# Kernel optimization log

Measured on AMD Instinct MI355X. Metric: run time of the kernel, lower is better.

## Reference

```python
import jax, jax.numpy as jnp
import numpy as np

N, F_IN, F_OUT, K = 4096, 32, 32, 2
NEG_SLOPE = 0.2
MASK_VAL = -9e15


def _sparse_mat(kv, km, density=0.01):
    vals = jax.random.normal(kv, (N, N), dtype=jnp.float32)
    mask = jax.random.uniform(km, (N, N)) < density
    return vals * mask


def setup_inputs() -> dict:
    key = jax.random.key(0)
    ks = jax.random.split(key, 12)
    x = jax.random.normal(ks[0], (N, F_IN), dtype=jnp.float32)
    Ld = _sparse_mat(ks[1], ks[2])
    Lu = _sparse_mat(ks[3], ks[4])
    P = jax.random.normal(ks[5], (N, N), dtype=jnp.float32) / np.sqrt(N)
    W1 = jax.random.normal(ks[6], (K, F_IN, F_OUT), dtype=jnp.float32) * 0.1
    W2 = jax.random.normal(ks[7], (K, F_IN, F_OUT), dtype=jnp.float32) * 0.1
    W0 = jax.random.normal(ks[8], (F_IN, F_OUT), dtype=jnp.float32) * 0.1
    att1 = jax.random.normal(ks[9], (2 * F_OUT * K, 1), dtype=jnp.float32) * 0.1
    att2 = jax.random.normal(ks[10], (2 * F_OUT * K, 1), dtype=jnp.float32) * 0.1
    return {"x": x, "Ld": Ld, "Lu": Lu, "P": P, "W1": W1, "W2": W2,
            "W0": W0, "att1": att1, "att2": att2}


def _branch(x, L, W, att):
    # W: [K, F_in, F_out]; precompute x @ W[k] for all k -> [K, N, F_out]
    Kk, _, Fo = W.shape
    xw = jnp.einsum('nf,kfo->kno', x, W)
    # torch.cat([x@W[k]], dim=1) == transpose+reshape of xw
    xcat = jnp.transpose(xw, (1, 0, 2)).reshape(x.shape[0], Kk * Fo)
    d = Fo * Kk
    e = xcat @ att[:d] + (xcat @ att[d:]).T            # [N, N]
    e = jax.nn.leaky_relu(e, negative_slope=NEG_SLOPE)
    e = jnp.where(L != 0, e, MASK_VAL)
    alpha = jax.nn.softmax(e, axis=1)                   # row softmax, no dropout (eval)
    z = alpha @ xw[0]
    a = alpha
    for k in range(1, Kk):
        a = a @ L
        z = z + a @ xw[k]
    return z


def reference(x, Ld, Lu, P, W1, W2, W0, att1, att2):
    z1 = _branch(x, Ld, W1, att1)
    z2 = _branch(x, Lu, W2, att2)
    x0 = P @ (x @ W0)
    return z1 + z2 + x0
```

## Files before the change

### kernel.cpp

```cpp
#include <hip/hip_runtime.h>
#include <hip/hip_bf16.h>

#define NN 4096
#define CAP 128
#define KS 8

typedef __attribute__((ext_vector_type(8))) short bf16x8;
typedef __attribute__((ext_vector_type(4))) float f32x4;

__device__ __forceinline__ float lrelu(float v) { return v >= 0.f ? v : 0.2f * v; }

__device__ __forceinline__ ushort f2bu(float f) {
    unsigned u = __float_as_uint(f);
    return (ushort)((u + 0x7FFFu + ((u >> 16) & 1u)) >> 16);
}

__global__ __launch_bounds__(256) void k_prep(
    const float* __restrict__ x,
    const float* __restrict__ W1, const float* __restrict__ W2,
    const float* __restrict__ W0,
    const float* __restrict__ att1, const float* __restrict__ att2,
    float* __restrict__ xwA1, float* __restrict__ xwB1,
    float* __restrict__ xwA2, float* __restrict__ xwB2,
    float* __restrict__ a1, float* __restrict__ b1,
    float* __restrict__ a2, float* __restrict__ b2,
    __hip_bfloat16* __restrict__ Bt)
{
    __shared__ float wl[5120];
    __shared__ float xs[256];
    const int t = threadIdx.x;
    for (int i = t; i < 2048; i += 256) { wl[i] = W1[i]; wl[2048 + i] = W2[i]; }
    for (int i = t; i < 1024; i += 256) wl[4096 + i] = W0[i];
    const int rowBase = blockIdx.x * 8;
    xs[t] = x[rowBase * 32 + t];
    __syncthreads();

    const int o = t & 31, r = t >> 5;
    const int row = rowBase + r;
    const float* xr = &xs[r * 32];
    float vA1 = 0.f, vB1 = 0.f, vA2 = 0.f, vB2 = 0.f, v0 = 0.f;
#pragma unroll
    for (int f = 0; f < 32; ++f) {
        const float xv = xr[f];
        vA1 += xv * wl[f * 32 + o];
        vB1 += xv * wl[1024 + f * 32 + o];
        vA2 += xv * wl[2048 + f * 32 + o];
        vB2 += xv * wl[3072 + f * 32 + o];
        v0  += xv * wl[4096 + f * 32 + o];
    }
    xwA1[row * 32 + o] = vA1;
    xwB1[row * 32 + o] = vB1;
    xwA2[row * 32 + o] = vA2;
    xwB2[row * 32 + o] = vB2;
    ((ushort*)Bt)[(size_t)o * NN + row] = f2bu(v0);

    float pa1 = vA1 * att1[o]      + vB1 * att1[32 + o];
    float pb1 = vA1 * att1[64 + o] + vB1 * att1[96 + o];
    float pa2 = vA2 * att2[o]      + vB2 * att2[32 + o];
    float pb2 = vA2 * att2[64 + o] + vB2 * att2[96 + o];
#pragma unroll
    for (int m = 1; m <= 16; m <<= 1) {
        pa1 += __shfl_xor(pa1, m); pb1 += __shfl_xor(pb1, m);
        pa2 += __shfl_xor(pa2, m); pb2 += __shfl_xor(pb2, m);
    }
    if (o == 0) { a1[row] = pa1; b1[row] = pb1; a2[row] = pa2; b2[row] = pb2; }
}

__global__ __launch_bounds__(256) void k_csr2(
    const float* __restrict__ Ld, const float* __restrict__ Lu,
    int2* __restrict__ csrv, int* __restrict__ cntArr)
{
    const int r0 = blockIdx.x * 2;
    const int t = threadIdx.x, lane = t & 63, w = t >> 6;
    __shared__ int wcnt[16];

    float4 v[16];
    {
        const float4* A0 = (const float4*)(Ld + (size_t)r0 * NN);
        const float4* B0 = (const float4*)(Lu + (size_t)r0 * NN);
        const float4* A1 = (const float4*)(Ld + (size_t)(r0 + 1) * NN);
        const float4* B1 = (const float4*)(Lu + (size_t)(r0 + 1) * NN);
#pragma unroll
        for (int it = 0; it < 4; ++it) {
            v[it]      = A0[it * 256 + t];
            v[4 + it]  = B0[it * 256 + t];
            v[8 + it]  = A1[it * 256 + t];
            v[12 + it] = B1[it * 256 + t];
        }
    }

    const unsigned long long lt = (1ull << lane) - 1ull;
#pragma unroll
    for (int c = 0; c < 4; ++c) {
        const int row = r0 + (c >> 1);
        const int br  = c & 1;
        int2* out = csrv + ((size_t)br * NN + row) * CAP;
        int tots[4];
#pragma unroll
        for (int it = 0; it < 4; ++it) {
            const float4 fv = v[c * 4 + it];
            tots[it] = __popcll(__ballot(fv.x != 0.f)) + __popcll(__ballot(fv.y != 0.f))
                     + __popcll(__ballot(fv.z != 0.f)) + __popcll(__ballot(fv.w != 0.f));
        }
        __syncthreads();
        if (lane == 0) {
            int4 tv; tv.x = tots[0]; tv.y = tots[1]; tv.z = tots[2]; tv.w = tots[3];
            *(int4*)&wcnt[w * 4] = tv;
        }
        __syncthreads();
        const int4 ca = *(const int4*)&wcnt[0];
        const int4 cb = *(const int4*)&wcnt[4];
        const int4 cc = *(const int4*)&wcnt[8];
        const int4 cd = *(const int4*)&wcnt[12];
        const int cs[16] = {ca.x, ca.y, ca.z, ca.w, cb.x, cb.y, cb.z, cb.w,
                            cc.x, cc.y, cc.z, cc.w, cd.x, cd.y, cd.z, cd.w};
        int total = 0;
#pragma unroll
        for (int k2 = 0; k2 < 16; ++k2) total += cs[k2];
        int base = 0;
#pragma unroll
        for (int k2 = 0; k2 < 16; ++k2) base += (k2 < (w << 2)) ? cs[k2] : 0;
        const int cnt  = min(total, CAP);
        const int cp16 = min((cnt + 15) & ~15, CAP);

#pragma unroll
        for (int it = 0; it < 4; ++it) {
            const float4 fv = v[c * 4 + it];
            const unsigned long long m0 = __ballot(fv.x != 0.f);
            const unsigned long long m1 = __ballot(fv.y != 0.f);
            const unsigned long long m2 = __ballot(fv.z != 0.f);
            const unsigned long long m3 = __ballot(fv.w != 0.f);
            const int p0 = __popcll(m0), p1 = __popcll(m1), p2 = __popcll(m2);
            const int c0 = (it * 256 + t) * 4;
            int s;
            s = base + __popcll(m0 & lt);
            if (fv.x != 0.f && s < CAP) { int2 e; e.x = c0;     e.y = __float_as_int(fv.x); out[s] = e; }
            s = base + p0 + __popcll(m1 & lt);
            if (fv.y != 0.f && s < CAP) { int2 e; e.x = c0 + 1; e.y = __float_as_int(fv.y); out[s] = e; }
            s = base + p0 + p1 + __popcll(m2 & lt);
            if (fv.z != 0.f && s < CAP) { int2 e; e.x = c0 + 2; e.y = __float_as_int(fv.z); out[s] = e; }
            s = base + p0 + p1 + p2 + __popcll(m3 & lt);
            if (fv.w != 0.f && s < CAP) { int2 e; e.x = c0 + 3; e.y = __float_as_int(fv.w); out[s] = e; }
            base += p0 + p1 + p2 + __popcll(m3);
        }
        if (t >= cnt && t < cp16) { int2 e; e.x = 0; e.y = 0; out[t] = e; }
        if (t == 0) cntArr[br * NN + row] = cnt;
    }
}

__global__ __launch_bounds__(256) void k_gather2(
    int2* __restrict__ csrv, const int* __restrict__ cntArr,
    const float* __restrict__ xwB1, const float* __restrict__ xwB2,
    const float* __restrict__ xwA1, const float* __restrict__ xwA2,
    const float* __restrict__ a1, const float* __restrict__ b1,
    const float* __restrict__ a2, const float* __restrict__ b2,
    float* __restrict__ u1, float* __restrict__ u2)
{
    __shared__ int2 sle[4][CAP];
    const int w = threadIdx.x >> 6, lane = threadIdx.x & 63;
    const int row = blockIdx.x * 4 + w;
    const int br  = blockIdx.y;
    const float* xwB = br ? xwB2 : xwB1;
    const float* xwA = br ? xwA2 : xwA1;
    const float* aA  = br ? a2 : a1;
    const float* bA  = br ? b2 : b1;
    float* u = br ? u2 : u1;

    const int cnt  = cntArr[br * NN + row];
    const int cp16 = min((cnt + 15) & ~15, CAP);
    int2* ci = csrv + ((size_t)br * NN + row) * CAP;
    int2* se = sle[w];
    int2 l0 = {0, 0}, l1 = {0, 0};
    if (lane < cp16)      { l0 = ci[lane];      se[lane]      = l0; }
    if (lane + 64 < cp16) { l1 = ci[lane + 64]; se[lane + 64] = l1; }

    const float ai = aA[row];
    const float e0 = (lane < cnt)      ? lrelu(ai + bA[l0.x]) : -1e30f;
    const float e1 = (lane + 64 < cnt) ? lrelu(ai + bA[l1.x]) : -1e30f;
    float lmax = fmaxf(e0, e1);
#pragma unroll
    for (int m = 1; m <= 32; m <<= 1) lmax = fmaxf(lmax, __shfl_xor(lmax, m));
    const float w0 = __expf(e0 - lmax), w1 = __expf(e1 - lmax);
    float ssum = w0 + w1;
#pragma unroll
    for (int m = 1; m <= 32; m <<= 1) ssum += __shfl_xor(ssum, m);
    const float inv = (cnt > 0) ? 1.f / ssum : 0.f;
    if (lane < cp16)      { l0.y = __float_as_int((lane < cnt)      ? w0 * inv : 0.f); ci[lane]      = l0; }
    if (lane + 64 < cp16) { l1.y = __float_as_int((lane + 64 < cnt) ? w1 * inv : 0.f); ci[lane + 64] = l1; }

    const int o = lane & 31, g = lane >> 5;
    float acc = 0.f;
    const int nb = cp16 >> 3;
    for (int j = 0; j < nb; ++j) {
        float wv[4], xv[4];
#pragma unroll
        for (int q = 0; q < 4; ++q) {
            const int2 e = se[8 * j + 2 * q + g];
            wv[q] = __int_as_float(e.y);
            xv[q] = xwB[(size_t)e.x * 32 + o];
        }
#pragma unroll
        for (int q = 0; q < 4; ++q) acc += wv[q] * xv[q];
    }
    acc += __shfl_xor(acc, 32);
    if (lane < 32) u[(size_t)row * 32 + o] = acc + xwA[(size_t)row * 32 + o];
}

__global__ __launch_bounds__(256) void k_accum(
    const int2* __restrict__ csrv, const int* __restrict__ cntArr,
    const float* __restrict__ u1, const float* __restrict__ u2,
    const float* __restrict__ partial, float* __restrict__ outp)
{
    __shared__ int2 sle[4][2 * CAP];
    const int w = threadIdx.x >> 6, lane = threadIdx.x & 63;
    const int row = blockIdx.x * 4 + w;
    const int o = lane & 31, g = lane >> 5;
    int2* se = sle[w];
    float total = 0.f;

    int cp[2];
#pragma unroll
    for (int br = 0; br < 2; ++br) {
        const int cnt = cntArr[br * NN + row];
        cp[br] = min((cnt + 15) & ~15, CAP);
        const int2* ci = csrv + ((size_t)br * NN + row) * CAP;
        if (lane < cp[br])      se[br * CAP + lane]      = ci[lane];
        if (lane + 64 < cp[br]) se[br * CAP + lane + 64] = ci[lane + 64];
    }

#pragma unroll
    for (int br = 0; br < 2; ++br) {
        const float* U = br ? u2 : u1;
        float acc = 0.f;
        const int nb = cp[br] >> 3;
        for (int j = 0; j < nb; ++j) {
            float wv[4], uv[4];
#pragma unroll
            for (int q = 0; q < 4; ++q) {
                const int2 e = se[br * CAP + 8 * j + 2 * q + g];
                wv[q] = __int_as_float(e.y);
                uv[q] = U[(size_t)e.x * 32 + o];
            }
#pragma unroll
            for (int q = 0; q < 4; ++q) acc += wv[q] * uv[q];
        }
        acc += __shfl_xor(acc, 32);
        total += acc;
    }

    if (lane < 32) {
#pragma unroll
        for (int p = 0; p < KS; ++p)
            total += partial[(size_t)p * NN * 32 + (size_t)row * 32 + o];
        outp[(size_t)row * 32 + o] = total;
    }
}

__global__ __launch_bounds__(256) void k_pgemm(
    const float* __restrict__ P, const ushort* __restrict__ Bt,
    float* __restrict__ partial)
{
    __shared__ ushort sA[2][16 * 64 * 8];
    __shared__ ushort sB[2][8 * 64 * 8];
    const int t = threadIdx.x;
    const int row0 = blockIdx.x * 64;
    const int ks = blockIdx.y;
    const float4*  P4  = (const float4*)P;
    const ushort4* Bt4 = (const ushort4*)Bt;

    const int lane = t & 63, w = t >> 6;

    f32x4 acc0 = {0.f, 0.f, 0.f, 0.f};
    f32x4 acc1 = {0.f, 0.f, 0.f, 0.f};

    auto stageA = [&](int c, int buf) {
        const int kc4 = (ks * 512 + c * 128) >> 2;
#pragma unroll
        for (int j = 0; j < 8; ++j) {
            const int i = t + 256 * j;
            const int row = i >> 5, q = i & 31;
            const float4 v = P4[(size_t)(row0 + row) * 1024 + kc4 + q];
            ushort4 u;
            u.x = f2bu(v.x); u.y = f2bu(v.y); u.z = f2bu(v.z); u.w = f2bu(v.w);
            const int wi = row >> 4, m = row & 15;
            const int kk = q >> 3, quad = (q >> 1) & 3, jj = q & 1;
            *(ushort4*)&sA[buf][(((wi * 4 + kk) * 64) + quad * 16 + m) * 8 + jj * 4] = u;
        }
    };
    auto stageB = [&](int c, int buf) {
        const int kc4 = (ks * 512 + c * 128) >> 2;
#pragma unroll
        for (int j = 0; j < 4; ++j) {
            const int i = t + 256 * j;
            const int o = i >> 5, q = i & 31;
            const ushort4 u = Bt4[(size_t)o * 1024 + kc4 + q];
            const int nt = o >> 4, n = o & 15;
            const int kk = q >> 3, quad = (q >> 1) & 3, jj = q & 1;
            *(ushort4*)&sB[buf][(((kk * 2 + nt) * 64) + quad * 16 + n) * 8 + jj * 4] = u;
        }
    };
    auto compute = [&](int buf) {
        const ushort* pa = &sA[buf][(w * 4) * 64 * 8 + lane * 8];
        const ushort* pb = &sB[buf][lane * 8];
#pragma unroll
        for (int kk = 0; kk < 4; ++kk) {
            const bf16x8 a  = *(const bf16x8*)(pa + kk * 512);
            const bf16x8 b0 = *(const bf16x8*)(pb + kk * 1024);
            const bf16x8 b1 = *(const bf16x8*)(pb + kk * 1024 + 512);
            acc0 = __builtin_amdgcn_mfma_f32_16x16x32_bf16(a, b0, acc0, 0, 0, 0);
            acc1 = __builtin_amdgcn_mfma_f32_16x16x32_bf16(a, b1, acc1, 0, 0, 0);
        }
    };

    stageA(0, 0); stageB(0, 0);
    __syncthreads();
    for (int c = 0; c < 4; ++c) {
        if (c < 3) { stageA(c + 1, (c + 1) & 1); stageB(c + 1, (c + 1) & 1); }
        compute(c & 1);
        __syncthreads();
    }

    const int m = lane & 15, quad = lane >> 4;
    float* out = partial + ((size_t)ks * NN + row0 + w * 16 + quad * 4) * 32;
#pragma unroll
    for (int r = 0; r < 4; ++r) {
        out[r * 32 + m]      = acc0[r];
        out[r * 32 + 16 + m] = acc1[r];
    }
}

extern "C" void kernel_launch(void* const* d_in, const int* in_sizes, int n_in,
                              void* d_out, int out_size, void* d_ws, size_t ws_size,
                              hipStream_t stream) {
    (void)in_sizes; (void)n_in; (void)out_size; (void)ws_size;
    const float* x    = (const float*)d_in[0];
    const float* Ld   = (const float*)d_in[1];
    const float* Lu   = (const float*)d_in[2];
    const float* P    = (const float*)d_in[3];
    const float* W1   = (const float*)d_in[4];
    const float* W2   = (const float*)d_in[5];
    const float* W0   = (const float*)d_in[6];
    const float* att1 = (const float*)d_in[7];
    const float* att2 = (const float*)d_in[8];

    float* ws = (float*)d_ws;
    float* xwA1 = ws;
    float* xwB1 = ws + 131072;
    float* xwA2 = ws + 262144;
    float* xwB2 = ws + 393216;
    float* u1   = ws + 524288;
    float* u2   = ws + 655360;
    float* a1   = ws + 786432;
    float* b1   = ws + 790528;
    float* a2   = ws + 794624;
    float* b2   = ws + 798720;
    float* partial = ws + 802816;
    __hip_bfloat16* Bt = (__hip_bfloat16*)(ws + 1851392);
    int2* csrv = (int2*)(ws + 1916928);
    int*  cnt  = (int*)(ws + 4014080);

    k_prep<<<512, 256, 0, stream>>>(x, W1, W2, W0, att1, att2,
                                    xwA1, xwB1, xwA2, xwB2, a1, b1, a2, b2, Bt);
    k_csr2<<<NN / 2, 256, 0, stream>>>(Ld, Lu, csrv, cnt);
    k_pgemm<<<dim3(64, KS), 256, 0, stream>>>(P, (const ushort*)Bt, partial);
    k_gather2<<<dim3(NN / 4, 2), 256, 0, stream>>>(csrv, cnt, xwB1, xwB2,
                                                   xwA1, xwA2, a1, b1, a2, b2,
                                                   u1, u2);
    k_accum<<<NN / 4, 256, 0, stream>>>(csrv, cnt, u1, u2, partial,
                                        (float*)d_out);
}
```

Baseline: 236.9 us.

## Fuse CSR compaction with softmax and gather into a single per-row kernel

```diff
diff --git a/kernel.cpp b/kernel.cpp
--- a/kernel.cpp
+++ b/kernel.cpp
@@ -66,144 +66,139 @@
     if (o == 0) { a1[row] = pa1; b1[row] = pb1; a2[row] = pa2; b2[row] = pb2; }
 }
 
-__global__ __launch_bounds__(256) void k_csr2(
+__global__ __launch_bounds__(256) void k_scan3(
     const float* __restrict__ Ld, const float* __restrict__ Lu,
-    int2* __restrict__ csrv, int* __restrict__ cntArr)
-{
-    const int r0 = blockIdx.x * 2;
-    const int t = threadIdx.x, lane = t & 63, w = t >> 6;
-    __shared__ int wcnt[16];
-
-    float4 v[16];
-    {
-        const float4* A0 = (const float4*)(Ld + (size_t)r0 * NN);
-        const float4* B0 = (const float4*)(Lu + (size_t)r0 * NN);
-        const float4* A1 = (const float4*)(Ld + (size_t)(r0 + 1) * NN);
-        const float4* B1 = (const float4*)(Lu + (size_t)(r0 + 1) * NN);
-#pragma unroll
-        for (int it = 0; it < 4; ++it) {
-            v[it]      = A0[it * 256 + t];
-            v[4 + it]  = B0[it * 256 + t];
-            v[8 + it]  = A1[it * 256 + t];
-            v[12 + it] = B1[it * 256 + t];
-        }
-    }
-
-    const unsigned long long lt = (1ull << lane) - 1ull;
-#pragma unroll
-    for (int c = 0; c < 4; ++c) {
-        const int row = r0 + (c >> 1);
-        const int br  = c & 1;
-        int2* out = csrv + ((size_t)br * NN + row) * CAP;
-        int tots[4];
-#pragma unroll
-        for (int it = 0; it < 4; ++it) {
-            const float4 fv = v[c * 4 + it];
-            tots[it] = __popcll(__ballot(fv.x != 0.f)) + __popcll(__ballot(fv.y != 0.f))
-                     + __popcll(__ballot(fv.z != 0.f)) + __popcll(__ballot(fv.w != 0.f));
-        }
-        __syncthreads();
-        if (lane == 0) {
-            int4 tv; tv.x = tots[0]; tv.y = tots[1]; tv.z = tots[2]; tv.w = tots[3];
-            *(int4*)&wcnt[w * 4] = tv;
-        }
-        __syncthreads();
-        const int4 ca = *(const int4*)&wcnt[0];
-        const int4 cb = *(const int4*)&wcnt[4];
-        const int4 cc = *(const int4*)&wcnt[8];
-        const int4 cd = *(const int4*)&wcnt[12];
-        const int cs[16] = {ca.x, ca.y, ca.z, ca.w, cb.x, cb.y, cb.z, cb.w,
-                            cc.x, cc.y, cc.z, cc.w, cd.x, cd.y, cd.z, cd.w};
-        int total = 0;
-#pragma unroll
-        for (int k2 = 0; k2 < 16; ++k2) total += cs[k2];
-        int base = 0;
-#pragma unroll
-        for (int k2 = 0; k2 < 16; ++k2) base += (k2 < (w << 2)) ? cs[k2] : 0;
-        const int cnt  = min(total, CAP);
-        const int cp16 = min((cnt + 15) & ~15, CAP);
-
-#pragma unroll
-        for (int it = 0; it < 4; ++it) {
-            const float4 fv = v[c * 4 + it];
-            const unsigned long long m0 = __ballot(fv.x != 0.f);
-            const unsigned long long m1 = __ballot(fv.y != 0.f);
-            const unsigned long long m2 = __ballot(fv.z != 0.f);
-            const unsigned long long m3 = __ballot(fv.w != 0.f);
-            const int p0 = __popcll(m0), p1 = __popcll(m1), p2 = __popcll(m2);
-            const int c0 = (it * 256 + t) * 4;
-            int s;
-            s = base + __popcll(m0 & lt);
-            if (fv.x != 0.f && s < CAP) { int2 e; e.x = c0;     e.y = __float_as_int(fv.x); out[s] = e; }
-            s = base + p0 + __popcll(m1 & lt);
-            if (fv.y != 0.f && s < CAP) { int2 e; e.x = c0 + 1; e.y = __float_as_int(fv.y); out[s] = e; }
-            s = base + p0 + p1 + __popcll(m2 & lt);
-            if (fv.z != 0.f && s < CAP) { int2 e; e.x = c0 + 2; e.y = __float_as_int(fv.z); out[s] = e; }
-            s = base + p0 + p1 + p2 + __popcll(m3 & lt);
-            if (fv.w != 0.f && s < CAP) { int2 e; e.x = c0 + 3; e.y = __float_as_int(fv.w); out[s] = e; }
-            base += p0 + p1 + p2 + __popcll(m3);
-        }
-        if (t >= cnt && t < cp16) { int2 e; e.x = 0; e.y = 0; out[t] = e; }
-        if (t == 0) cntArr[br * NN + row] = cnt;
-    }
-}
-
-__global__ __launch_bounds__(256) void k_gather2(
-    int2* __restrict__ csrv, const int* __restrict__ cntArr,
     const float* __restrict__ xwB1, const float* __restrict__ xwB2,
     const float* __restrict__ xwA1, const float* __restrict__ xwA2,
     const float* __restrict__ a1, const float* __restrict__ b1,
     const float* __restrict__ a2, const float* __restrict__ b2,
+    int2* __restrict__ csrv, int* __restrict__ cntArr,
     float* __restrict__ u1, float* __restrict__ u2)
 {
-    __shared__ int2 sle[4][CAP];
-    const int w = threadIdx.x >> 6, lane = threadIdx.x & 63;
-    const int row = blockIdx.x * 4 + w;
+    const int row = blockIdx.x;
     const int br  = blockIdx.y;
+    const float* L   = br ? Lu : Ld;
     const float* xwB = br ? xwB2 : xwB1;
     const float* xwA = br ? xwA2 : xwA1;
     const float* aA  = br ? a2 : a1;
     const float* bA  = br ? b2 : b1;
-    float* u = br ? u2 : u1;
-
-    const int cnt  = cntArr[br * NN + row];
+    int2* csrB = csrv + ((size_t)br * NN + row) * CAP;
+    float* u   = br ? u2 : u1;
+
+    __shared__ int   sidx[CAP];
+    __shared__ float sval[CAP];
+    __shared__ int   wcnt[16];
+    __shared__ float red[256];
+    __shared__ float rpart[8];
+    const int t = threadIdx.x;
+    const int lane = t & 63, w = t >> 6;
+
+    const float4* L4 = (const float4*)(L + (size_t)row * NN);
+    float4 v[4];
+#pragma unroll
+    for (int it = 0; it < 4; ++it) v[it] = L4[it * 256 + t];
+
+    const unsigned long long lt = (1ull << lane) - 1ull;
+
+    int tots[4];
+#pragma unroll
+    for (int it = 0; it < 4; ++it) {
+        const unsigned long long m0 = __ballot(v[it].x != 0.f);
+        const unsigned long long m1 = __ballot(v[it].y != 0.f);
+        const unsigned long long m2 = __ballot(v[it].z != 0.f);
+        const unsigned long long m3 = __ballot(v[it].w != 0.f);
+        tots[it] = __popcll(m0) + __popcll(m1) + __popcll(m2) + __popcll(m3);
+    }
+    if (lane == 0) {
+        int4 tv; tv.x = tots[0]; tv.y = tots[1]; tv.z = tots[2]; tv.w = tots[3];
+        *(int4*)&wcnt[w * 4] = tv;
+    }
+    __syncthreads();
+
+    const int4 ca = *(const int4*)&wcnt[0];
+    const int4 cb = *(const int4*)&wcnt[4];
+    const int4 cc = *(const int4*)&wcnt[8];
+    const int4 cd = *(const int4*)&wcnt[12];
+    const int cs[16] = {ca.x, ca.y, ca.z, ca.w, cb.x, cb.y, cb.z, cb.w,
+                        cc.x, cc.y, cc.z, cc.w, cd.x, cd.y, cd.z, cd.w};
+    int total = 0;
+#pragma unroll
+    for (int k2 = 0; k2 < 16; ++k2) total += cs[k2];
+    int base = 0;
+#pragma unroll
+    for (int k2 = 0; k2 < 16; ++k2) base += (k2 < (w << 2)) ? cs[k2] : 0;
+
+    const int cnt  = min(total, CAP);
     const int cp16 = min((cnt + 15) & ~15, CAP);
-    int2* ci = csrv + ((size_t)br * NN + row) * CAP;
-    int2* se = sle[w];
-    int2 l0 = {0, 0}, l1 = {0, 0};
-    if (lane < cp16)      { l0 = ci[lane];      se[lane]      = l0; }
-    if (lane + 64 < cp16) { l1 = ci[lane + 64]; se[lane + 64] = l1; }
+
+#pragma unroll
+    for (int it = 0; it < 4; ++it) {
+        const float vx = v[it].x, vy = v[it].y, vz = v[it].z, vw = v[it].w;
+        const unsigned long long m0 = __ballot(vx != 0.f);
+        const unsigned long long m1 = __ballot(vy != 0.f);
+        const unsigned long long m2 = __ballot(vz != 0.f);
+        const unsigned long long m3 = __ballot(vw != 0.f);
+        const int p0 = __popcll(m0), p1 = __popcll(m1), p2 = __popcll(m2);
+        const int c0 = (it * 256 + t) * 4;
+        int s;
+        s = base + __popcll(m0 & lt);
+        if (vx != 0.f && s < CAP) { sidx[s] = c0;     sval[s] = vx; }
+        s = base + p0 + __popcll(m1 & lt);
+        if (vy != 0.f && s < CAP) { sidx[s] = c0 + 1; sval[s] = vy; }
+        s = base + p0 + p1 + __popcll(m2 & lt);
+        if (vz != 0.f && s < CAP) { sidx[s] = c0 + 2; sval[s] = vz; }
+        s = base + p0 + p1 + p2 + __popcll(m3 & lt);
+        if (vw != 0.f && s < CAP) { sidx[s] = c0 + 3; sval[s] = vw; }
+        base += p0 + p1 + p2 + __popcll(m3);
+    }
+    if (t >= cnt && t < cp16) { sidx[t] = 0; sval[t] = 0.f; }
+    __syncthreads();
 
     const float ai = aA[row];
-    const float e0 = (lane < cnt)      ? lrelu(ai + bA[l0.x]) : -1e30f;
-    const float e1 = (lane + 64 < cnt) ? lrelu(ai + bA[l1.x]) : -1e30f;
-    float lmax = fmaxf(e0, e1);
-#pragma unroll
-    for (int m = 1; m <= 32; m <<= 1) lmax = fmaxf(lmax, __shfl_xor(lmax, m));
-    const float w0 = __expf(e0 - lmax), w1 = __expf(e1 - lmax);
-    float ssum = w0 + w1;
-#pragma unroll
-    for (int m = 1; m <= 32; m <<= 1) ssum += __shfl_xor(ssum, m);
+    const int myidx = (t < cp16) ? sidx[t] : 0;
+    const float e = (t < cnt) ? lrelu(ai + bA[myidx]) : -1e30f;
+    float m = e;
+#pragma unroll
+    for (int mm = 1; mm <= 32; mm <<= 1) m = fmaxf(m, __shfl_xor(m, mm));
+    if (lane == 0) rpart[w] = m;
+    __syncthreads();
+    m = fmaxf(fmaxf(rpart[0], rpart[1]), fmaxf(rpart[2], rpart[3]));
+    const float wgt = (t < cnt) ? __expf(e - m) : 0.f;
+    float ss = wgt;
+#pragma unroll
+    for (int mm = 1; mm <= 32; mm <<= 1) ss += __shfl_xor(ss, mm);
+    if (lane == 0) rpart[4 + w] = ss;
+    __syncthreads();
+    const float ssum = rpart[4] + rpart[5] + rpart[6] + rpart[7];
     const float inv = (cnt > 0) ? 1.f / ssum : 0.f;
-    if (lane < cp16)      { l0.y = __float_as_int((lane < cnt)      ? w0 * inv : 0.f); ci[lane]      = l0; }
-    if (lane + 64 < cp16) { l1.y = __float_as_int((lane + 64 < cnt) ? w1 * inv : 0.f); ci[lane + 64] = l1; }
-
-    const int o = lane & 31, g = lane >> 5;
+    if (t < cp16) { int2 eo; eo.x = myidx; eo.y = __float_as_int(wgt * inv); csrB[t] = eo; }
+    if (t == 0) cntArr[br * NN + row] = cnt;
+
+    const int o = t & 31, g = t >> 5;
     float acc = 0.f;
-    const int nb = cp16 >> 3;
-    for (int j = 0; j < nb; ++j) {
-        float wv[4], xv[4];
-#pragma unroll
-        for (int q = 0; q < 4; ++q) {
-            const int2 e = se[8 * j + 2 * q + g];
-            wv[q] = __int_as_float(e.y);
-            xv[q] = xwB[(size_t)e.x * 32 + o];
-        }
-#pragma unroll
-        for (int q = 0; q < 4; ++q) acc += wv[q] * xv[q];
-    }
-    acc += __shfl_xor(acc, 32);
-    if (lane < 32) u[(size_t)row * 32 + o] = acc + xwA[(size_t)row * 32 + o];
+    const int nPair = cp16 >> 4;
+    if (nPair > 0) {
+        float vA0 = sval[g],      vA1 = sval[g + 8];
+        float xA0 = xwB[(size_t)sidx[g] * 32 + o];
+        float xA1 = xwB[(size_t)sidx[g + 8] * 32 + o];
+        for (int j = 1; j < nPair; ++j) {
+            const int sB = g + 16 * j;
+            const float vB0 = sval[sB],  vB1 = sval[sB + 8];
+            const float xB0 = xwB[(size_t)sidx[sB] * 32 + o];
+            const float xB1 = xwB[(size_t)sidx[sB + 8] * 32 + o];
+            acc += vA0 * xA0 + vA1 * xA1;
+            vA0 = vB0; xA0 = xB0; vA1 = vB1; xA1 = xB1;
+        }
+        acc += vA0 * xA0 + vA1 * xA1;
+    }
+    red[t] = acc;
+    __syncthreads();
+    if (t < 32) {
+        float tot2 = 0.f;
+#pragma unroll
+        for (int g2 = 0; g2 < 8; ++g2) tot2 += red[g2 * 32 + t];
+        u[(size_t)row * 32 + t] = tot2 + xwA[(size_t)row * 32 + t];
+    }
 }
 
 __global__ __launch_bounds__(256) void k_accum(
@@ -361,11 +356,9 @@
 
     k_prep<<<512, 256, 0, stream>>>(x, W1, W2, W0, att1, att2,
                                     xwA1, xwB1, xwA2, xwB2, a1, b1, a2, b2, Bt);
-    k_csr2<<<NN / 2, 256, 0, stream>>>(Ld, Lu, csrv, cnt);
+    k_scan3<<<dim3(NN, 2), 256, 0, stream>>>(Ld, Lu, xwB1, xwB2, xwA1, xwA2,
+                                             a1, b1, a2, b2, csrv, cnt, u1, u2);
     k_pgemm<<<dim3(64, KS), 256, 0, stream>>>(P, (const ushort*)Bt, partial);
-    k_gather2<<<dim3(NN / 4, 2), 256, 0, stream>>>(csrv, cnt, xwB1, xwB2,
-                                                   xwA1, xwA2, a1, b1, a2, b2,
-                                                   u1, u2);
     k_accum<<<NN / 4, 256, 0, stream>>>(csrv, cnt, u1, u2, partial,
                                         (float*)d_out);
 }
```

After: 224.0 us. -5.4%, faster.
